# Optimization experiments

Measured on AMD Instinct MI355X. Metric: run time of the kernel, lower is better.

The kernel has to match this reference:

```python
import jax, jax.numpy as jnp
import numpy as np

NUM_EMBEDDINGS = 1024
EMBEDDING_DIM = 64


def setup_inputs() -> dict:
    key = jax.random.key(0)
    k1, k2 = jax.random.split(key)
    z = jax.random.normal(k1, (64, 32, 32, EMBEDDING_DIM), dtype=jnp.float32)
    # torch init: uniform_(-1/num_embeddings, 1/num_embeddings)
    lim = 1.0 / NUM_EMBEDDINGS
    codebook = jax.random.uniform(
        k2, (NUM_EMBEDDINGS, EMBEDDING_DIM), dtype=jnp.float32,
        minval=-lim, maxval=lim)
    return {"z": z, "codebook": codebook}


def reference(z, codebook):
    # z: [..., D]; codebook: [K, D]
    z_flat = z.reshape(-1, z.shape[-1])                      # [N, D]
    # ||z||^2 - 2 z.e + ||e||^2  -> [N, K]
    distances = (
        jnp.sum(z_flat ** 2, axis=1, keepdims=True)
        - 2.0 * jnp.einsum("nd,kd->nk", z_flat, codebook)
        + jnp.sum(codebook ** 2, axis=1)
    )
    min_indices = jnp.argmin(distances, axis=1)              # [N]
    z_q = jnp.take(codebook, min_indices, axis=0).reshape(z.shape)
    return z_q, min_indices
```

## Files before the change

kernel.cpp:

```cpp
#include <hip/hip_runtime.h>
#include <hip/hip_bf16.h>
#include <math.h>


#define D      64
#define K      1024
#define BLOCK  256

typedef _Float16 half8_t __attribute__((ext_vector_type(8)));
typedef float    floatx4 __attribute__((ext_vector_type(4)));

#define WS_CN_OFF    0
#define WS_EF_OFF    4096

__device__ __forceinline__ void gld_lds16(const void* g, void* l) {
    __builtin_amdgcn_global_load_lds(
        (const __attribute__((address_space(1))) void*)g,
        (__attribute__((address_space(3))) void*)l, 16, 0, 0);
}

__device__ __forceinline__ float np_sumsq64_p(const float* __restrict__ x) {
    float r[8];
    {
        float4 v0 = *(const float4*)(x);
        float4 v1 = *(const float4*)(x + 4);
        r[0] = __fmul_rn(v0.x, v0.x); r[1] = __fmul_rn(v0.y, v0.y);
        r[2] = __fmul_rn(v0.z, v0.z); r[3] = __fmul_rn(v0.w, v0.w);
        r[4] = __fmul_rn(v1.x, v1.x); r[5] = __fmul_rn(v1.y, v1.y);
        r[6] = __fmul_rn(v1.z, v1.z); r[7] = __fmul_rn(v1.w, v1.w);
    }
#pragma unroll
    for (int i = 8; i < 64; i += 8) {
        float4 v0 = *(const float4*)(x + i);
        float4 v1 = *(const float4*)(x + i + 4);
        r[0] = __fadd_rn(r[0], __fmul_rn(v0.x, v0.x));
        r[1] = __fadd_rn(r[1], __fmul_rn(v0.y, v0.y));
        r[2] = __fadd_rn(r[2], __fmul_rn(v0.z, v0.z));
        r[3] = __fadd_rn(r[3], __fmul_rn(v0.w, v0.w));
        r[4] = __fadd_rn(r[4], __fmul_rn(v1.x, v1.x));
        r[5] = __fadd_rn(r[5], __fmul_rn(v1.y, v1.y));
        r[6] = __fadd_rn(r[6], __fmul_rn(v1.z, v1.z));
        r[7] = __fadd_rn(r[7], __fmul_rn(v1.w, v1.w));
    }
    return __fadd_rn(__fadd_rn(__fadd_rn(r[0], r[1]), __fadd_rn(r[2], r[3])),
                     __fadd_rn(__fadd_rn(r[4], r[5]), __fadd_rn(r[6], r[7])));
}

__global__ void vq_pre(const float* __restrict__ cb, float* __restrict__ cn,
                       _Float16* __restrict__ ef) {
    const int k = blockIdx.x * 64 + threadIdx.x;
    if (k >= K) return;
    cn[k] = np_sumsq64_p(cb + (long)k * D);
    const int t = k >> 6, ct = (k >> 4) & 3, l16 = k & 15;
#pragma unroll
    for (int ch = 0; ch < 2; ++ch)
#pragma unroll
        for (int quad = 0; quad < 4; ++quad) {
            const float* p = cb + (long)k * D + ch * 32 + quad * 8;
            half8_t h1, h2;
#pragma unroll
            for (int j = 0; j < 8; ++j) {
                float x10 = __fmul_rn(p[j], 1024.0f);
                _Float16 g1 = (_Float16)x10;
                h1[j] = g1;
                h2[j] = (_Float16)(__fmul_rn(__fsub_rn(x10, (float)g1), 2048.0f));
            }
            const int base = t * 8192 + 128 * quad + 8 * l16;
            *(half8_t*)(ef + base + 512 * (ch * 4 + ct))       = h1;
            *(half8_t*)(ef + base + 512 * ((2 + ch) * 4 + ct)) = h2;
        }
}

__global__ __launch_bounds__(BLOCK, 2) void vq_main(
    const float* __restrict__ z, const float* __restrict__ cb,
    const _Float16* __restrict__ ef, const float* __restrict__ cn,
    float* __restrict__ zq, float* __restrict__ idx_out) {
    __shared__ __align__(16) char smem[34816];
    __shared__ float sS[128];
    __shared__ float sCn[K];
    __shared__ int   sBi[128];
    float*    zf   = (float*)smem;
    _Float16* bufs = (_Float16*)smem;

    const int tid  = threadIdx.x;
    const int lane = tid & 63;
    const int wv   = tid >> 6;
    const int quad = lane >> 4;
    const int l16  = lane & 15;
    const long rowbase = (long)blockIdx.x * 128;

    const float4* gz = (const float4*)(z + rowbase * D);
#pragma unroll
    for (int i = 0; i < 8; ++i) {
        int idx4 = i * BLOCK + tid;
        int r = idx4 >> 4, j = idx4 & 15;
        *(float4*)(zf + r * 68 + j * 4) = gz[idx4];
    }
#pragma unroll
    for (int i = 0; i < 4; ++i) sCn[i * 256 + tid] = cn[i * 256 + tid];
    __syncthreads();

    if (tid < 128) sS[tid] = np_sumsq64_p(zf + tid * 68);

    half8_t a1[2][2], a2[2][2];
#pragma unroll
    for (int rt = 0; rt < 2; ++rt) {
        const int row = wv * 32 + rt * 16 + l16;
#pragma unroll
        for (int ch = 0; ch < 2; ++ch) {
            const float* p = zf + row * 68 + ch * 32 + quad * 8;
            float4 f0 = *(const float4*)(p);
            float4 f1 = *(const float4*)(p + 4);
            float xs[8] = {f0.x, f0.y, f0.z, f0.w, f1.x, f1.y, f1.z, f1.w};
#pragma unroll
            for (int j = 0; j < 8; ++j) {
                _Float16 h1 = (_Float16)xs[j];
                a1[rt][ch][j] = h1;
                a2[rt][ch][j] =
                    (_Float16)(__fmul_rn(__fsub_rn(xs[j], (float)h1), 2048.0f));
            }
        }
    }
    __syncthreads();

    float myS[2][4];
#pragma unroll
    for (int rt = 0; rt < 2; ++rt)
#pragma unroll
        for (int r = 0; r < 4; ++r)
            myS[rt][r] = sS[wv * 32 + rt * 16 + quad * 4 + r];

    float bv[2][4];
    int   bi[2][4];
#pragma unroll
    for (int rt = 0; rt < 2; ++rt)
#pragma unroll
        for (int r = 0; r < 4; ++r) { bv[rt][r] = INFINITY; bi[rt][r] = 0; }

    const char* eb = (const char*)ef;

    {
        const char* g = eb + wv * 4096 + lane * 16;
        char* l = (char*)bufs + wv * 4096;
#pragma unroll
        for (int i = 0; i < 4; ++i) gld_lds16(g + i * 1024, l + i * 1024);
    }
    __syncthreads();

    for (int t = 0; t < 16; ++t) {
        const _Float16* cur = bufs + (t & 1) * 8192;
        if (t < 15) {
            const char* g = eb + (t + 1) * 16384 + wv * 4096 + lane * 16;
            char* l = (char*)bufs + ((t + 1) & 1) * 16384 + wv * 4096;
#pragma unroll
            for (int i = 0; i < 4; ++i) gld_lds16(g + i * 1024, l + i * 1024);
        }

        const _Float16* tb = cur + 8 * lane;
        const int kbase = t * 64;
#pragma unroll
        for (int ct = 0; ct < 4; ++ct) {
            half8_t b1[2], b2[2];
#pragma unroll
            for (int ch = 0; ch < 2; ++ch) {
                b1[ch] = *(const half8_t*)(tb + 512 * (ch * 4 + ct));
                b2[ch] = *(const half8_t*)(tb + 512 * ((2 + ch) * 4 + ct));
            }
            const float cnv = sCn[kbase + ct * 16 + l16];
            const int kg = kbase + ct * 16 + l16;
#pragma unroll
            for (int rt = 0; rt < 2; ++rt) {
                floatx4 aM = (floatx4){0.f, 0.f, 0.f, 0.f};
                floatx4 aC = (floatx4){0.f, 0.f, 0.f, 0.f};
                aM = __builtin_amdgcn_mfma_f32_16x16x32_f16(a1[rt][0], b1[0], aM, 0, 0, 0);
                aM = __builtin_amdgcn_mfma_f32_16x16x32_f16(a1[rt][1], b1[1], aM, 0, 0, 0);
                aC = __builtin_amdgcn_mfma_f32_16x16x32_f16(a1[rt][0], b2[0], aC, 0, 0, 0);
                aC = __builtin_amdgcn_mfma_f32_16x16x32_f16(a1[rt][1], b2[1], aC, 0, 0, 0);
                aC = __builtin_amdgcn_mfma_f32_16x16x32_f16(a2[rt][0], b1[0], aC, 0, 0, 0);
                aC = __builtin_amdgcn_mfma_f32_16x16x32_f16(a2[rt][1], b1[1], aC, 0, 0, 0);
#pragma unroll
                for (int r = 0; r < 4; ++r) {
                    float ds = fmaf(aC[r], 0x1p-11f, aM[r]);
                    float t2 = __fmul_rn(ds, 0x1p-9f);
                    float dist = __fadd_rn(__fsub_rn(myS[rt][r], t2), cnv);
                    if (dist < bv[rt][r]) { bv[rt][r] = dist; bi[rt][r] = kg; }
                }
            }
        }
        __syncthreads();
    }

#pragma unroll
    for (int rt = 0; rt < 2; ++rt)
#pragma unroll
        for (int r = 0; r < 4; ++r) {
            float v = bv[rt][r];
            int   x = bi[rt][r];
#pragma unroll
            for (int off = 1; off <= 8; off <<= 1) {
                float ov = __shfl_xor(v, off);
                int   ox = __shfl_xor(x, off);
                if (ov < v || (ov == v && ox < x)) { v = ov; x = ox; }
            }
            if (l16 == 0) {
                const int rl = wv * 32 + rt * 16 + quad * 4 + r;
                sBi[rl] = x;
                idx_out[rowbase + rl] = (float)x;
            }
        }
    __syncthreads();

    const float4* cb4 = (const float4*)cb;
    float4* zq4 = (float4*)(zq + rowbase * D);
#pragma unroll
    for (int i = 0; i < 8; ++i) {
        int idx4 = i * BLOCK + tid;
        int r = idx4 >> 4, j = idx4 & 15;
        zq4[idx4] = cb4[(long)sBi[r] * 16 + j];
    }
}

extern "C" void kernel_launch(void* const* d_in, const int* in_sizes, int n_in,
                              void* d_out, int out_size, void* d_ws, size_t ws_size,
                              hipStream_t stream) {
    const float* z  = (const float*)d_in[0];
    const float* cb = (const float*)d_in[1];

    const int n_rows = in_sizes[0] / D;
    float* zq      = (float*)d_out;
    float* idx_out = zq + (long)n_rows * D;

    float*    ws_cn = (float*)((char*)d_ws + WS_CN_OFF);
    _Float16* ws_ef = (_Float16*)((char*)d_ws + WS_EF_OFF);

    vq_pre<<<K / 64, 64, 0, stream>>>(cb, ws_cn, ws_ef);
    vq_main<<<n_rows / 128, BLOCK, 0, stream>>>(z, cb, ws_ef, ws_cn, zq, idx_out);
}
```

Before: 101.1 us.

## Keep codebook slices register-resident per wave and pack argmin into double keys

The block grows to 1024 threads (16 waves). Each wave now holds its own 64-entry slice of the split-fp16 codebook in registers and loops over the block's 128 rows, where before every wave streamed the whole codebook through double-buffered LDS with a barrier per tile. The row fragments are converted to hi/lo fp16 once into LDS and shared by all waves. Distance and index are packed into one double so a single fmin does the argmin with a lowest-index tie-break, and the 16 per-wave partial minima are merged through LDS. The cost is more registers per thread, one block of 1024 threads per CU, and an extra cross-wave merge step.

```diff
diff --git a/kernel.cpp b/kernel.cpp
--- a/kernel.cpp
+++ b/kernel.cpp
@@ -5,19 +5,13 @@
 
 #define D      64
 #define K      1024
-#define BLOCK  256
 
 typedef _Float16 half8_t __attribute__((ext_vector_type(8)));
 typedef float    floatx4 __attribute__((ext_vector_type(4)));
-
-#define WS_CN_OFF    0
-#define WS_EF_OFF    4096
-
-__device__ __forceinline__ void gld_lds16(const void* g, void* l) {
-    __builtin_amdgcn_global_load_lds(
-        (const __attribute__((address_space(1))) void*)g,
-        (__attribute__((address_space(3))) void*)l, 16, 0, 0);
-}
+typedef unsigned long long u64;
+
+#define WS_CN_OFF 0
+#define WS_EF_OFF 4096
 
 __device__ __forceinline__ float np_sumsq64_p(const float* __restrict__ x) {
     float r[8];
@@ -71,16 +65,15 @@
         }
 }
 
-__global__ __launch_bounds__(BLOCK, 2) void vq_main(
+__global__ __launch_bounds__(1024) void vq_main(
     const float* __restrict__ z, const float* __restrict__ cb,
     const _Float16* __restrict__ ef, const float* __restrict__ cn,
     float* __restrict__ zq, float* __restrict__ idx_out) {
-    __shared__ __align__(16) char smem[34816];
+    __shared__ __align__(16) float    zf[128 * 68];
+    __shared__ __align__(16) _Float16 za[8 * 2048];
     __shared__ float sS[128];
-    __shared__ float sCn[K];
+    __shared__ u64   smerge[128 * 18];
     __shared__ int   sBi[128];
-    float*    zf   = (float*)smem;
-    _Float16* bufs = (_Float16*)smem;
 
     const int tid  = threadIdx.x;
     const int lane = tid & 63;
@@ -89,134 +82,116 @@
     const int l16  = lane & 15;
     const long rowbase = (long)blockIdx.x * 128;
 
+    const _Float16* myef = ef + wv * 8192;
+    half8_t b1[4][2], b2[4][2];
+#pragma unroll
+    for (int ct = 0; ct < 4; ++ct)
+#pragma unroll
+        for (int ch = 0; ch < 2; ++ch) {
+            b1[ct][ch] = *(const half8_t*)(myef + 512 * (ch * 4 + ct) + 8 * lane);
+            b2[ct][ch] = *(const half8_t*)(myef + 512 * ((2 + ch) * 4 + ct) + 8 * lane);
+        }
+    const int kl = wv * 64 + l16;
+    float mycn[4];
+#pragma unroll
+    for (int ct = 0; ct < 4; ++ct) mycn[ct] = cn[kl + ct * 16];
+
     const float4* gz = (const float4*)(z + rowbase * D);
 #pragma unroll
-    for (int i = 0; i < 8; ++i) {
-        int idx4 = i * BLOCK + tid;
+    for (int i = 0; i < 2; ++i) {
+        int idx4 = i * 1024 + tid;
         int r = idx4 >> 4, j = idx4 & 15;
         *(float4*)(zf + r * 68 + j * 4) = gz[idx4];
     }
-#pragma unroll
-    for (int i = 0; i < 4; ++i) sCn[i * 256 + tid] = cn[i * 256 + tid];
-    __syncthreads();
-
-    if (tid < 128) sS[tid] = np_sumsq64_p(zf + tid * 68);
-
-    half8_t a1[2][2], a2[2][2];
-#pragma unroll
-    for (int rt = 0; rt < 2; ++rt) {
-        const int row = wv * 32 + rt * 16 + l16;
+    __syncthreads();
+
+    if (lane < 8) sS[wv * 8 + lane] = np_sumsq64_p(zf + (wv * 8 + lane) * 68);
+
+    {
+        const int t = wv >> 1, spl = wv & 1;
 #pragma unroll
         for (int ch = 0; ch < 2; ++ch) {
-            const float* p = zf + row * 68 + ch * 32 + quad * 8;
+            const float* p = zf + (t * 16 + l16) * 68 + ch * 32 + quad * 8;
             float4 f0 = *(const float4*)(p);
             float4 f1 = *(const float4*)(p + 4);
             float xs[8] = {f0.x, f0.y, f0.z, f0.w, f1.x, f1.y, f1.z, f1.w};
+            half8_t h;
 #pragma unroll
             for (int j = 0; j < 8; ++j) {
                 _Float16 h1 = (_Float16)xs[j];
-                a1[rt][ch][j] = h1;
-                a2[rt][ch][j] =
-                    (_Float16)(__fmul_rn(__fsub_rn(xs[j], (float)h1), 2048.0f));
-            }
-        }
-    }
-    __syncthreads();
-
-    float myS[2][4];
-#pragma unroll
-    for (int rt = 0; rt < 2; ++rt)
-#pragma unroll
-        for (int r = 0; r < 4; ++r)
-            myS[rt][r] = sS[wv * 32 + rt * 16 + quad * 4 + r];
-
-    float bv[2][4];
-    int   bi[2][4];
-#pragma unroll
-    for (int rt = 0; rt < 2; ++rt)
-#pragma unroll
-        for (int r = 0; r < 4; ++r) { bv[rt][r] = INFINITY; bi[rt][r] = 0; }
-
-    const char* eb = (const char*)ef;
+                h[j] = spl ? (_Float16)(__fmul_rn(__fsub_rn(xs[j], (float)h1), 2048.0f))
+                           : h1;
+            }
+            *(half8_t*)(za + t * 2048 + (spl * 2 + ch) * 512 + 8 * lane) = h;
+        }
+    }
+    __syncthreads();
+
+    const double INF_KEY = __builtin_bit_cast(double, 0x7F800000FFFFFFFFull);
+
+    for (int t = 0; t < 8; ++t) {
+        half8_t a1[2], a2[2];
+#pragma unroll
+        for (int ch = 0; ch < 2; ++ch) {
+            a1[ch] = *(const half8_t*)(za + t * 2048 + ch * 512 + 8 * lane);
+            a2[ch] = *(const half8_t*)(za + t * 2048 + (2 + ch) * 512 + 8 * lane);
+        }
+        float4 Sv4 = *(const float4*)(sS + t * 16 + quad * 4);
+        float Sarr[4] = {Sv4.x, Sv4.y, Sv4.z, Sv4.w};
+        double best[4] = {INF_KEY, INF_KEY, INF_KEY, INF_KEY};
+
+#pragma unroll
+        for (int ct = 0; ct < 4; ++ct) {
+            floatx4 aM = (floatx4){0.f, 0.f, 0.f, 0.f};
+            floatx4 aC = (floatx4){0.f, 0.f, 0.f, 0.f};
+#pragma unroll
+            for (int ch = 0; ch < 2; ++ch) {
+                aM = __builtin_amdgcn_mfma_f32_16x16x32_f16(a1[ch], b1[ct][ch], aM, 0, 0, 0);
+                aC = __builtin_amdgcn_mfma_f32_16x16x32_f16(a1[ch], b2[ct][ch], aC, 0, 0, 0);
+                aC = __builtin_amdgcn_mfma_f32_16x16x32_f16(a2[ch], b1[ct][ch], aC, 0, 0, 0);
+            }
+            const unsigned kg = (unsigned)(kl + ct * 16);
+#pragma unroll
+            for (int r = 0; r < 4; ++r) {
+                float ds = fmaf(aC[r], 0x1p-11f, aM[r]);
+                float t2 = __fmul_rn(ds, 0x1p-9f);
+                float dist = __fadd_rn(__fsub_rn(Sarr[r], t2), mycn[ct]);
+                uint2 u; u.x = kg; u.y = __float_as_uint(dist);
+                best[r] = fmin(best[r], __builtin_bit_cast(double, u));
+            }
+        }
+#pragma unroll
+        for (int r = 0; r < 4; ++r) {
+            double v = best[r];
+#pragma unroll
+            for (int off = 1; off <= 8; off <<= 1)
+                v = fmin(v, __shfl_xor(v, off));
+            if (l16 == 0)
+                smerge[(t * 16 + quad * 4 + r) * 18 + wv] = __builtin_bit_cast(u64, v);
+        }
+    }
+    __syncthreads();
+
+    if (lane < 8) {
+        const int row = wv * 8 + lane;
+        const u64* m = smerge + row * 18;
+        double v = __builtin_bit_cast(double, m[0]);
+#pragma unroll
+        for (int i = 1; i < 16; ++i)
+            v = fmin(v, __builtin_bit_cast(double, m[i]));
+        const unsigned kbest = (unsigned)(__builtin_bit_cast(u64, v) & 0xFFFFFFFFull);
+        sBi[row] = (int)kbest;
+        idx_out[rowbase + row] = (float)kbest;
+    }
+    __syncthreads();
 
     {
-        const char* g = eb + wv * 4096 + lane * 16;
-        char* l = (char*)bufs + wv * 4096;
-#pragma unroll
-        for (int i = 0; i < 4; ++i) gld_lds16(g + i * 1024, l + i * 1024);
-    }
-    __syncthreads();
-
-    for (int t = 0; t < 16; ++t) {
-        const _Float16* cur = bufs + (t & 1) * 8192;
-        if (t < 15) {
-            const char* g = eb + (t + 1) * 16384 + wv * 4096 + lane * 16;
-            char* l = (char*)bufs + ((t + 1) & 1) * 16384 + wv * 4096;
-#pragma unroll
-            for (int i = 0; i < 4; ++i) gld_lds16(g + i * 1024, l + i * 1024);
-        }
-
-        const _Float16* tb = cur + 8 * lane;
-        const int kbase = t * 64;
-#pragma unroll
-        for (int ct = 0; ct < 4; ++ct) {
-            half8_t b1[2], b2[2];
-#pragma unroll
-            for (int ch = 0; ch < 2; ++ch) {
-                b1[ch] = *(const half8_t*)(tb + 512 * (ch * 4 + ct));
-                b2[ch] = *(const half8_t*)(tb + 512 * ((2 + ch) * 4 + ct));
-            }
-            const float cnv = sCn[kbase + ct * 16 + l16];
-            const int kg = kbase + ct * 16 + l16;
-#pragma unroll
-            for (int rt = 0; rt < 2; ++rt) {
-                floatx4 aM = (floatx4){0.f, 0.f, 0.f, 0.f};
-                floatx4 aC = (floatx4){0.f, 0.f, 0.f, 0.f};
-                aM = __builtin_amdgcn_mfma_f32_16x16x32_f16(a1[rt][0], b1[0], aM, 0, 0, 0);
-                aM = __builtin_amdgcn_mfma_f32_16x16x32_f16(a1[rt][1], b1[1], aM, 0, 0, 0);
-                aC = __builtin_amdgcn_mfma_f32_16x16x32_f16(a1[rt][0], b2[0], aC, 0, 0, 0);
-                aC = __builtin_amdgcn_mfma_f32_16x16x32_f16(a1[rt][1], b2[1], aC, 0, 0, 0);
-                aC = __builtin_amdgcn_mfma_f32_16x16x32_f16(a2[rt][0], b1[0], aC, 0, 0, 0);
-                aC = __builtin_amdgcn_mfma_f32_16x16x32_f16(a2[rt][1], b1[1], aC, 0, 0, 0);
-#pragma unroll
-                for (int r = 0; r < 4; ++r) {
-                    float ds = fmaf(aC[r], 0x1p-11f, aM[r]);
-                    float t2 = __fmul_rn(ds, 0x1p-9f);
-                    float dist = __fadd_rn(__fsub_rn(myS[rt][r], t2), cnv);
-                    if (dist < bv[rt][r]) { bv[rt][r] = dist; bi[rt][r] = kg; }
-                }
-            }
-        }
-        __syncthreads();
-    }
-
-#pragma unroll
-    for (int rt = 0; rt < 2; ++rt)
-#pragma unroll
-        for (int r = 0; r < 4; ++r) {
-            float v = bv[rt][r];
-            int   x = bi[rt][r];
-#pragma unroll
-            for (int off = 1; off <= 8; off <<= 1) {
-                float ov = __shfl_xor(v, off);
-                int   ox = __shfl_xor(x, off);
-                if (ov < v || (ov == v && ox < x)) { v = ov; x = ox; }
-            }
-            if (l16 == 0) {
-                const int rl = wv * 32 + rt * 16 + quad * 4 + r;
-                sBi[rl] = x;
-                idx_out[rowbase + rl] = (float)x;
-            }
-        }
-    __syncthreads();
-
-    const float4* cb4 = (const float4*)cb;
-    float4* zq4 = (float4*)(zq + rowbase * D);
-#pragma unroll
-    for (int i = 0; i < 8; ++i) {
-        int idx4 = i * BLOCK + tid;
-        int r = idx4 >> 4, j = idx4 & 15;
-        zq4[idx4] = cb4[(long)sBi[r] * 16 + j];
+        const int row = tid >> 3, j = tid & 7;
+        const int kk = sBi[row];
+        const float4* src = (const float4*)(cb + (long)kk * D);
+        float4* dst = (float4*)(zq + (rowbase + row) * D);
+        dst[j * 2]     = src[j * 2];
+        dst[j * 2 + 1] = src[j * 2 + 1];
     }
 }
 
@@ -234,5 +209,5 @@
     _Float16* ws_ef = (_Float16*)((char*)d_ws + WS_EF_OFF);
 
     vq_pre<<<K / 64, 64, 0, stream>>>(cb, ws_cn, ws_ef);
-    vq_main<<<n_rows / 128, BLOCK, 0, stream>>>(z, cb, ws_ef, ws_cn, zq, idx_out);
-}
+    vq_main<<<n_rows / 128, 1024, 0, stream>>>(z, cb, ws_ef, ws_cn, zq, idx_out);
+}
```

Measured after the change: 115.6 us. +14.4%, slower.
